# Kernel optimization log

Hardware: AMD Instinct MI355X
Metric: run time of the kernel (lower is better)

The kernel has to match this reference:

```python
import jax, jax.numpy as jnp
import numpy as np

D = 768; NH = 12; HD = D // NH; L = 12; NC = 27; PATCH = 16; MLP = 3072; PROJ = 512
IMG = 224; GRID = IMG // PATCH; HW = GRID * GRID; S = NC + HW
NEG = -1e9

def _ln(x, w, b):
    m = jnp.mean(x, -1, keepdims=True)
    v = jnp.mean(jnp.square(x - m), -1, keepdims=True)
    return (x - m) * jax.lax.rsqrt(v + 1e-5) * w + b

def _quick_gelu(x):
    return x * jax.nn.sigmoid(1.702 * x)

def _build_mask(attn_obj_masks, dtype):
    # CRIS block mask: cls<->cls blocked except self; cls->patch allowed only for
    # patches of that class; patch->cls blocked; patch->patch fully allowed.
    B = attn_obj_masks.shape[0]
    oh = jax.nn.one_hot(attn_obj_masks, NC, dtype=dtype)              # [B, HW, NC]
    T11 = jnp.broadcast_to(1.0 - jnp.eye(NC, dtype=dtype), (B, NC, NC))
    M13 = 1.0 - jnp.swapaxes(oh, 1, 2)                                # [B, NC, HW]
    top = jnp.concatenate([T11, M13], axis=2)
    bot = jnp.concatenate([jnp.ones((B, HW, NC), dtype), jnp.zeros((B, HW, HW), dtype)], axis=2)
    Mb = jnp.concatenate([top, bot], axis=1)                          # [B, S, S]
    return jnp.where(Mb == 1.0, jnp.asarray(NEG, dtype), jnp.asarray(0.0, dtype))

def reference(img, sents, attn_obj_masks, obj_masks, cls_tokens, patch_w, patch_b, pos_embed,
              ln1_w, ln1_b, qkv_w, qkv_b, out_w, out_b, ln2_w, ln2_b,
              mlp_w1, mlp_b1, mlp_w2, mlp_b2, ln_post_w, ln_post_b, proj):
    B = img.shape[0]
    sents = sents / jnp.linalg.norm(sents, axis=-1, keepdims=True)    # encode_text output, L2 normed
    mask = _build_mask(attn_obj_masks, img.dtype)                     # [B, S, S]
    # patch embedding (conv stride 16) -> [B, HW, D]
    p = jax.lax.conv_general_dilated(img, patch_w, (PATCH, PATCH), 'VALID',
                                     dimension_numbers=('NCHW', 'OIHW', 'NCHW'))
    p = p.reshape(B, D, HW).transpose(0, 2, 1) + patch_b
    x = jnp.concatenate([jnp.broadcast_to(cls_tokens, (B, NC, D)), p], axis=1) + pos_embed
    scale = 1.0 / np.sqrt(HD).astype(np.float32)
    def block(x, prm):
        l1w, l1b, qw, qb, ow, ob, l2w, l2b, w1, b1, w2, b2 = prm
        h = _ln(x, l1w, l1b)
        qkv = h @ qw + qb
        q, k, v = jnp.split(qkv, 3, axis=-1)
        q = q.reshape(B, S, NH, HD).transpose(0, 2, 1, 3)
        k = k.reshape(B, S, NH, HD).transpose(0, 2, 1, 3)
        v = v.reshape(B, S, NH, HD).transpose(0, 2, 1, 3)
        scores = jnp.einsum('bhqd,bhkd->bhqk', q, k) * scale + mask[:, None]
        a = jax.nn.softmax(scores, axis=-1)
        o = jnp.einsum('bhqk,bhkd->bhqd', a, v).transpose(0, 2, 1, 3).reshape(B, S, D)
        x = x + o @ ow + ob
        h = _ln(x, l2w, l2b)
        x = x + _quick_gelu(h @ w1 + b1) @ w2 + b2
        return x, None
    x, _ = jax.lax.scan(block, x, (ln1_w, ln1_b, qkv_w, qkv_b, out_w, out_b,
                                   ln2_w, ln2_b, mlp_w1, mlp_b1, mlp_w2, mlp_b2))
    tokens = _ln(x, ln_post_w, ln_post_b) @ proj                      # [B, S, PROJ]
    obj = tokens[:, :NC]
    obj = obj / jnp.linalg.norm(obj, axis=-1, keepdims=True)
    pred_id = jnp.einsum('bnd,bd->bn', obj, sents)                    # [B, NC]
    # per-class scatter loop == gather of pred_id by per-pixel class id
    pred = jnp.take_along_axis(pred_id, obj_masks.reshape(B, -1), axis=1).reshape(obj_masks.shape)
    return pred                                                       # [B, 224, 224]

def setup_inputs():
    B = 16; std = 0.02
    ks = jax.random.split(jax.random.key(0), 16)
    f = jax.random.normal
    return {
        'img': f(ks[0], (B, 3, IMG, IMG), jnp.float32),
        'sents': f(ks[1], (B, PROJ), jnp.float32),
        'attn_obj_masks': jax.random.randint(ks[2], (B, HW), 0, NC, jnp.int32),
        'obj_masks': jax.random.randint(ks[3], (B, IMG, IMG), 0, NC, jnp.int32),
        'cls_tokens': f(ks[4], (1, NC, D)) * std,
        'patch_w': f(ks[5], (D, 3, PATCH, PATCH)) * std,
        'patch_b': jnp.zeros((D,)),
        'pos_embed': f(ks[6], (S, D)) * std,
        'ln1_w': jnp.ones((L, D)), 'ln1_b': jnp.zeros((L, D)),
        'qkv_w': f(ks[7], (L, D, 3 * D)) * std, 'qkv_b': jnp.zeros((L, 3 * D)),
        'out_w': f(ks[8], (L, D, D)) * std, 'out_b': jnp.zeros((L, D)),
        'ln2_w': jnp.ones((L, D)), 'ln2_b': jnp.zeros((L, D)),
        'mlp_w1': f(ks[9], (L, D, MLP)) * std, 'mlp_b1': jnp.zeros((L, MLP)),
        'mlp_w2': f(ks[10], (L, MLP, D)) * std, 'mlp_b2': jnp.zeros((L, D)),
        'ln_post_w': jnp.ones((D,)), 'ln_post_b': jnp.zeros((D,)),
        'proj': f(ks[11], (D, PROJ)) * std,
    }
```

## Files before the change

kernel.cpp:

```cpp
#include <hip/hip_runtime.h>

#define DEV __device__ __forceinline__

typedef short bf16x8 __attribute__((ext_vector_type(8)));
typedef float f32x4 __attribute__((ext_vector_type(4)));
typedef int vi4 __attribute__((ext_vector_type(4)));
typedef unsigned short u16;
typedef short short4v __attribute__((ext_vector_type(4)));

#define NEGV -1000000000.0f

DEV u16 f2bf(float f) {
  union { float f; unsigned u; } v; v.f = f;
  unsigned r = v.u + 0x7FFFu + ((v.u >> 16) & 1u);
  return (u16)(r >> 16);
}

DEV bf16x8 ld_bf8(const u16* p) {
  vi4 v = *(const vi4*)p;
  return __builtin_bit_cast(bf16x8, v);
}

DEV void gload_lds16(const u16* g, vi4* l) {
  __builtin_amdgcn_global_load_lds((const __attribute__((address_space(1))) void*)g,
                                   (__attribute__((address_space(3))) void*)l, 16, 0, 0);
}

template<int BN, int MODE, bool GELU, int KS>
__global__ __launch_bounds__(256) void gemm_bt(
    const u16* __restrict__ A, const u16* __restrict__ Bt,
    const float* __restrict__ bias,
    float* __restrict__ Cf, u16* __restrict__ Cb,
    int M, int N, int K, const float* __restrict__ pos)
{
  constexpr int FJ = BN / 32;
  constexpr int LTOT = 4 + FJ;
  __shared__ vi4 As[2][1024];
  __shared__ vi4 Bs[2][BN * 8];

  int gx = gridDim.x, gy = gridDim.y;
  int nwg = gx * gy * (int)gridDim.z;
  int orig = blockIdx.x + gx * (blockIdx.y + gy * blockIdx.z);
  int qq = nwg >> 3, rr = nwg & 7;
  int xcd = orig & 7, off = orig >> 3;
  int id = (xcd < rr) ? xcd * (qq + 1) + off : rr * (qq + 1) + (xcd - rr) * qq + off;
  int bx = id % gx, rest = id / gx, by = rest % gy, bz = rest / gy;

  int tid = threadIdx.x, lane = tid & 63, wid = tid >> 6;
  int wm = wid >> 1, wn = wid & 1;
  int m0 = by * 128, n0 = bx * BN;
  int kBeg = (K / KS) * bz;
  int nT = (K / KS) >> 6;
  f32x4 acc[4][FJ] = {};

  auto STAGE = [&](int buf, int kk) {
    #pragma unroll
    for (int r = 0; r < 4; ++r) {
      int flat = r * 256 + tid;
      int row = flat >> 3, c = flat & 7;
      int cs = c ^ (row & 7);
      gload_lds16(A + (long)(m0 + row) * K + kk + cs * 8, &As[buf][r * 256 + wid * 64]);
    }
    #pragma unroll
    for (int r = 0; r < FJ; ++r) {
      int flat = r * 256 + tid;
      int row = flat >> 3, c = flat & 7;
      int cs = c ^ (row & 7);
      gload_lds16(Bt + (long)(n0 + row) * K + kk + cs * 8, &Bs[buf][r * 256 + wid * 64]);
    }
  };

  STAGE(0, kBeg);
  int cur = 0;
  for (int t = 0; t < nT; ++t) {
    if (t + 1 < nT) {
      STAGE(cur ^ 1, kBeg + (t + 1) * 64);
      asm volatile("s_waitcnt vmcnt(%0)" :: "i"(LTOT) : "memory");
    } else {
      asm volatile("s_waitcnt vmcnt(0)" ::: "memory");
    }
    __builtin_amdgcn_s_barrier();
    int cg = lane >> 4, l15 = lane & 15;
    #pragma unroll
    for (int ks = 0; ks < 2; ++ks) {
      bf16x8 af[4], bfr[FJ];
      #pragma unroll
      for (int i = 0; i < 4; ++i) {
        int ra = wm * 64 + i * 16 + l15;
        af[i] = __builtin_bit_cast(bf16x8, As[cur][ra * 8 + ((ks * 4 + cg) ^ (ra & 7))]);
      }
      #pragma unroll
      for (int j = 0; j < FJ; ++j) {
        int rb = wn * (BN / 2) + j * 16 + l15;
        bfr[j] = __builtin_bit_cast(bf16x8, Bs[cur][rb * 8 + ((ks * 4 + cg) ^ (rb & 7))]);
      }
      #pragma unroll
      for (int i = 0; i < 4; ++i)
        #pragma unroll
        for (int j = 0; j < FJ; ++j)
          acc[i][j] = __builtin_amdgcn_mfma_f32_16x16x32_bf16(af[i], bfr[j], acc[i][j], 0, 0, 0);
    }
    __builtin_amdgcn_s_barrier();
    cur ^= 1;
  }

  int cg = lane >> 4, l15 = lane & 15;
  #pragma unroll
  for (int i = 0; i < 4; ++i) {
    #pragma unroll
    for (int j = 0; j < FJ; ++j) {
      int col = n0 + wn * (BN / 2) + j * 16 + l15;
      float bv = bias ? bias[col] : 0.f;
      #pragma unroll
      for (int r = 0; r < 4; ++r) {
        int row = m0 + wm * 64 + i * 16 + cg * 4 + r;
        if (row < M) {
          float v = acc[i][j][r];
          if (KS == 1 || bz == 0) v += bv;
          if (GELU) v = v / (1.f + __expf(-1.702f * v));
          if (MODE == 0) Cb[(long)row * N + col] = f2bf(v);
          else if (MODE == 1) {
            if (KS > 1) atomicAdd(&Cf[(long)row * N + col], v);
            else Cf[(long)row * N + col] += v;
          }
          else if (MODE == 2) Cf[(long)row * N + col] = v;
          else {
            int hw = row % 196;
            int xr = (row / 196) * 223 + 27 + hw;
            Cf[(long)xr * 768 + col] = v + pos[(27 + hw) * 768 + col];
          }
        }
      }
    }
  }
}

__global__ __launch_bounds__(256) void attn_kernel(
    const u16* __restrict__ QKV, const int* __restrict__ aom, u16* __restrict__ O)
{
  __shared__ vi4 Kl[224 * 8];
  __shared__ vi4 Vt[64 * 28];
  __shared__ vi4 Pl[4][16 * 28];
  __shared__ int ml[196];
  int tid = threadIdx.x, lane = tid & 63, wid = tid >> 6;
  int qg = blockIdx.x, h = blockIdx.y, b = blockIdx.z;
  long rowbase = (long)b * 223;
  #pragma unroll
  for (int it = 0; it < 7; ++it) {
    int flat = it * 256 + tid;
    int s = flat >> 3, c = flat & 7;
    int cs = c ^ (s & 7);
    gload_lds16(QKV + (rowbase + s) * 2304 + 768 + h * 64 + cs * 8, &Kl[it * 256 + wid * 64]);
  }
  u16* vt16 = (u16*)Vt;
  #pragma unroll
  for (int it = 0; it < 7; ++it) {
    int flat = it * 256 + tid;
    int s = flat >> 3, c = flat & 7;
    vi4 v = {0, 0, 0, 0};
    if (s < 223) v = *(const vi4*)(QKV + (rowbase + s) * 2304 + 1536 + h * 64 + c * 8);
    union { vi4 v4; u16 hx[8]; } uu; uu.v4 = v;
    int cs = s >> 3;
    #pragma unroll
    for (int j = 0; j < 8; ++j) {
      int d = c * 8 + j;
      vt16[d * 224 + (cs ^ ((d >> 1) & 3)) * 8 + (s & 7)] = uu.hx[j];
    }
  }
  for (int i = tid; i < 196; i += 256) ml[i] = aom[b * 196 + i];
  __syncthreads();

  int colk = lane & 15, cg = lane >> 4;
  #pragma unroll
  for (int rep = 0; rep < 2; ++rep) {
    int fo = wid * 2 + rep;
    if (fo >= 7) break;
    int qf = qg * 7 + fo;
    int q0 = qf * 16;
    int arow = q0 + colk; if (arow > 222) arow = 222;
    const u16* qb = QKV + (rowbase + arow) * 2304 + h * 64;
    bf16x8 aq0 = ld_bf8(qb + cg * 8);
    bf16x8 aq1 = ld_bf8(qb + 32 + cg * 8);

    f32x4 sc[14];
    #pragma unroll
    for (int kf = 0; kf < 14; ++kf) {
      int key = kf * 16 + colk;
      f32x4 a = {0.f, 0.f, 0.f, 0.f};
      bf16x8 bk0 = __builtin_bit_cast(bf16x8, Kl[key * 8 + (cg ^ (key & 7))]);
      bf16x8 bk1 = __builtin_bit_cast(bf16x8, Kl[key * 8 + ((4 + cg) ^ (key & 7))]);
      a = __builtin_amdgcn_mfma_f32_16x16x32_bf16(aq0, bk0, a, 0, 0, 0);
      a = __builtin_amdgcn_mfma_f32_16x16x32_bf16(aq1, bk1, a, 0, 0, 0);
      sc[kf] = a;
    }
    #pragma unroll
    for (int r = 0; r < 4; ++r) {
      int q = q0 + cg * 4 + r;
      float mx = -3.4e38f;
      #pragma unroll
      for (int kf = 0; kf < 14; ++kf) {
        int key = kf * 16 + colk;
        float mval;
        if (key >= 223) mval = NEGV;
        else if (q >= 27) mval = (key < 27) ? NEGV : 0.f;
        else if (key < 27) mval = (key == q) ? 0.f : NEGV;
        else mval = (ml[key - 27] == q) ? 0.f : NEGV;
        float s = sc[kf][r] * 0.125f + mval;
        sc[kf][r] = s;
        mx = fmaxf(mx, s);
      }
      #pragma unroll
      for (int d = 1; d < 16; d <<= 1) mx = fmaxf(mx, __shfl_xor(mx, d));
      float sum = 0.f;
      #pragma unroll
      for (int kf = 0; kf < 14; ++kf) {
        float e = __expf(sc[kf][r] - mx);
        sc[kf][r] = e; sum += e;
      }
      #pragma unroll
      for (int d = 1; d < 16; d <<= 1) sum += __shfl_xor(sum, d);
      float inv = 1.f / sum;
      #pragma unroll
      for (int kf = 0; kf < 14; ++kf) sc[kf][r] *= inv;
    }
    u16* pw = (u16*)Pl[wid];
    #pragma unroll
    for (int kf = 0; kf < 14; ++kf) {
      int key = kf * 16 + colk;
      int ck = key >> 3;
      #pragma unroll
      for (int r = 0; r < 4; ++r) {
        int prow = cg * 4 + r;
        pw[prow * 224 + (ck ^ ((prow >> 1) & 3)) * 8 + (key & 7)] = f2bf(sc[kf][r]);
      }
    }
    f32x4 oacc[4] = {};
    #pragma unroll
    for (int ks = 0; ks < 7; ++ks) {
      bf16x8 pa = __builtin_bit_cast(bf16x8, Pl[wid][colk * 28 + ((ks * 4 + cg) ^ ((colk >> 1) & 3))]);
      #pragma unroll
      for (int nf = 0; nf < 4; ++nf) {
        int d = nf * 16 + colk;
        bf16x8 bv = __builtin_bit_cast(bf16x8, Vt[d * 28 + ((ks * 4 + cg) ^ ((d >> 1) & 3))]);
        oacc[nf] = __builtin_amdgcn_mfma_f32_16x16x32_bf16(pa, bv, oacc[nf], 0, 0, 0);
      }
    }
    #pragma unroll
    for (int nf = 0; nf < 4; ++nf) {
      int d = h * 64 + nf * 16 + colk;
      #pragma unroll
      for (int r = 0; r < 4; ++r) {
        int q = q0 + cg * 4 + r;
        if (q < 223) O[(rowbase + q) * 768 + d] = f2bf(oacc[nf][r]);
      }
    }
  }
}

template<bool MAP27>
__global__ __launch_bounds__(256) void ln_kernel(
    const float* __restrict__ X, u16* __restrict__ Hb,
    const float* __restrict__ w, const float* __restrict__ bb, int nrows)
{
  int row = blockIdx.x * 4 + (threadIdx.x >> 6);
  if (row >= nrows) return;
  int xr = MAP27 ? (row / 27) * 223 + (row % 27) : row;
  int l = threadIdx.x & 63;
  const float4* xp = (const float4*)(X + (long)xr * 768);
  float4 a = xp[l], c = xp[l + 64], d = xp[l + 128];
  float s = a.x + a.y + a.z + a.w + c.x + c.y + c.z + c.w + d.x + d.y + d.z + d.w;
  #pragma unroll
  for (int t = 1; t < 64; t <<= 1) s += __shfl_xor(s, t);
  float mean = s * (1.f / 768.f);
  a.x -= mean; a.y -= mean; a.z -= mean; a.w -= mean;
  c.x -= mean; c.y -= mean; c.z -= mean; c.w -= mean;
  d.x -= mean; d.y -= mean; d.z -= mean; d.w -= mean;
  float q = a.x*a.x + a.y*a.y + a.z*a.z + a.w*a.w
          + c.x*c.x + c.y*c.y + c.z*c.z + c.w*c.w
          + d.x*d.x + d.y*d.y + d.z*d.z + d.w*d.w;
  #pragma unroll
  for (int t = 1; t < 64; t <<= 1) q += __shfl_xor(q, t);
  float rs = rsqrtf(q * (1.f / 768.f) + 1e-5f);
  const float4* wp = (const float4*)w;
  const float4* bp = (const float4*)bb;
  u16* out = Hb + (long)row * 768;
  float4 w0 = wp[l], w1 = wp[l + 64], w2 = wp[l + 128];
  float4 b0 = bp[l], b1 = bp[l + 64], b2 = bp[l + 128];
  short4v o;
  o[0] = (short)f2bf(a.x * rs * w0.x + b0.x); o[1] = (short)f2bf(a.y * rs * w0.y + b0.y);
  o[2] = (short)f2bf(a.z * rs * w0.z + b0.z); o[3] = (short)f2bf(a.w * rs * w0.w + b0.w);
  *(short4v*)(out + l * 4) = o;
  o[0] = (short)f2bf(c.x * rs * w1.x + b1.x); o[1] = (short)f2bf(c.y * rs * w1.y + b1.y);
  o[2] = (short)f2bf(c.z * rs * w1.z + b1.z); o[3] = (short)f2bf(c.w * rs * w1.w + b1.w);
  *(short4v*)(out + 256 + l * 4) = o;
  o[0] = (short)f2bf(d.x * rs * w2.x + b2.x); o[1] = (short)f2bf(d.y * rs * w2.y + b2.y);
  o[2] = (short)f2bf(d.z * rs * w2.z + b2.z); o[3] = (short)f2bf(d.w * rs * w2.w + b2.w);
  *(short4v*)(out + 512 + l * 4) = o;
}

__global__ __launch_bounds__(256) void transpose_w(
    const float* __restrict__ W, u16* __restrict__ WT, int K, int N, long sW, long sT)
{
  __shared__ float t[64][65];
  int z = blockIdx.z;
  W += (long)z * sW; WT += (long)z * sT;
  int n0 = blockIdx.x * 64, k0 = blockIdx.y * 64;
  #pragma unroll
  for (int i = 0; i < 4; ++i) {
    int flat = i * 256 + threadIdx.x;
    int r = flat >> 4, c = (flat & 15) * 4;
    float4 v = *(const float4*)(W + (long)(k0 + r) * N + n0 + c);
    t[r][c] = v.x; t[r][c + 1] = v.y; t[r][c + 2] = v.z; t[r][c + 3] = v.w;
  }
  __syncthreads();
  #pragma unroll
  for (int i = 0; i < 8; ++i) {
    int flat = i * 256 + threadIdx.x;
    int rn = flat >> 5, ck = (flat & 31) * 2;
    unsigned val = (unsigned)f2bf(t[ck][rn]) | ((unsigned)f2bf(t[ck + 1][rn]) << 16);
    *(unsigned*)(WT + (long)(n0 + rn) * K + k0 + ck) = val;
  }
}

__global__ void convert_bf16(const float* __restrict__ src, u16* __restrict__ dst, int n) {
  int i = blockIdx.x * 256 + threadIdx.x;
  if (i < n) dst[i] = f2bf(src[i]);
}

__global__ __launch_bounds__(192) void patch_extract(const float* __restrict__ img, u16* __restrict__ Xp) {
  int row = blockIdx.x;
  int t = threadIdx.x;
  int pair = t >> 2, part = t & 3;
  int cch = pair >> 4, kh = pair & 15;
  int b = row / 196, hw = row % 196, gh = hw / 14, gw = hw % 14;
  float4 v = *(const float4*)(img + ((long)(b * 3 + cch) * 224 + gh * 16 + kh) * 224 + gw * 16 + part * 4);
  short4v o;
  o[0] = (short)f2bf(v.x); o[1] = (short)f2bf(v.y); o[2] = (short)f2bf(v.z); o[3] = (short)f2bf(v.w);
  *(short4v*)(Xp + (long)row * 768 + pair * 16 + part * 4) = o;
}

__global__ void cls_pos_fill(const float* __restrict__ cls, const float* __restrict__ pos, float* __restrict__ x) {
  int i = blockIdx.x * 256 + threadIdx.x;
  if (i >= 16 * 27 * 768) return;
  int d = i % 768, t = i / 768, b = t / 27, s = t % 27;
  x[((long)b * 223 + s) * 768 + d] = cls[s * 768 + d] + pos[s * 768 + d];
}

__global__ __launch_bounds__(256) void sents_norm(const float* __restrict__ s, float* __restrict__ sn) {
  __shared__ float sb[4];
  int b = blockIdx.x, t = threadIdx.x;
  float v0 = s[b * 512 + t], v1 = s[b * 512 + t + 256];
  float q = v0 * v0 + v1 * v1;
  #pragma unroll
  for (int d = 1; d < 64; d <<= 1) q += __shfl_xor(q, d);
  if ((t & 63) == 0) sb[t >> 6] = q;
  __syncthreads();
  float inv = rsqrtf(sb[0] + sb[1] + sb[2] + sb[3]);
  sn[b * 512 + t] = v0 * inv;
  sn[b * 512 + t + 256] = v1 * inv;
}

__global__ __launch_bounds__(256) void obj_dot(const float* __restrict__ obj, const float* __restrict__ sn, float* __restrict__ pid) {
  __shared__ float sb[8];
  int r = blockIdx.x, t = threadIdx.x, b = r / 27;
  float v0 = obj[(long)r * 512 + t], v1 = obj[(long)r * 512 + t + 256];
  float w0 = sn[b * 512 + t], w1 = sn[b * 512 + t + 256];
  float q = v0 * v0 + v1 * v1;
  float dt = v0 * w0 + v1 * w1;
  #pragma unroll
  for (int d = 1; d < 64; d <<= 1) { q += __shfl_xor(q, d); dt += __shfl_xor(dt, d); }
  if ((t & 63) == 0) { sb[t >> 6] = q; sb[4 + (t >> 6)] = dt; }
  __syncthreads();
  if (t == 0) pid[r] = (sb[4] + sb[5] + sb[6] + sb[7]) * rsqrtf(sb[0] + sb[1] + sb[2] + sb[3]);
}

__global__ void gather_pred(const int* __restrict__ om, const float* __restrict__ pid, float* __restrict__ out) {
  int i = blockIdx.x * 256 + threadIdx.x;
  if (i >= 16 * 224 * 224) return;
  int b = i / (224 * 224);
  out[i] = pid[b * 27 + om[i]];
}

extern "C" void kernel_launch(void* const* d_in, const int* in_sizes, int n_in,
                              void* d_out, int out_size, void* d_ws, size_t ws_size,
                              hipStream_t stream) {
  const float* img     = (const float*)d_in[0];
  const float* sents   = (const float*)d_in[1];
  const int*   aom     = (const int*)d_in[2];
  const int*   omask   = (const int*)d_in[3];
  const float* cls     = (const float*)d_in[4];
  const float* patch_w = (const float*)d_in[5];
  const float* patch_b = (const float*)d_in[6];
  const float* pos     = (const float*)d_in[7];
  const float* ln1w    = (const float*)d_in[8];
  const float* ln1b    = (const float*)d_in[9];
  const float* qkvw    = (const float*)d_in[10];
  const float* qkvb    = (const float*)d_in[11];
  const float* outw    = (const float*)d_in[12];
  const float* outb    = (const float*)d_in[13];
  const float* ln2w    = (const float*)d_in[14];
  const float* ln2b    = (const float*)d_in[15];
  const float* m1w     = (const float*)d_in[16];
  const float* m1b     = (const float*)d_in[17];
  const float* m2w     = (const float*)d_in[18];
  const float* m2b     = (const float*)d_in[19];
  const float* lnpw    = (const float*)d_in[20];
  const float* lnpb    = (const float*)d_in[21];
  const float* projw   = (const float*)d_in[22];

  char* p = (char*)d_ws;
  auto alloc = [&](size_t bytes) { char* r = p; p += (bytes + 255) & ~(size_t)255; return r; };
  float* x   = (float*)alloc(3568ul * 768 * 4);
  u16* H     = (u16*)alloc(3584ul * 768 * 2);
  u16* QKV   = (u16*)alloc(3584ul * 2304 * 2);
  u16* Obuf  = (u16*)alloc(3584ul * 768 * 2);
  u16* G     = (u16*)alloc(3584ul * 3072 * 2);
  u16* PWc   = (u16*)alloc(768ul * 768 * 2);
  u16* PrT   = (u16*)alloc(512ul * 768 * 2);
  float* obj = (float*)alloc(432ul * 512 * 4);
  float* sn  = (float*)alloc(16ul * 512 * 4);
  float* pid = (float*)alloc(432ul * 4);

  const size_t wlayer = (2304ul * 768 + 768ul * 768 + 3072ul * 768 + 768ul * 3072) * 2;
  size_t used = (size_t)(p - (char*)d_ws);
  int nw = (ws_size >= used + 12 * wlayer + 65536) ? 12 : 1;
  const long sQ = 2304l * 768, sO = 768l * 768, s1 = 768l * 3072, s2 = 3072l * 768;
  u16* WqT = (u16*)alloc((size_t)sQ * 2 * nw);
  u16* WoT = (u16*)alloc((size_t)sO * 2 * nw);
  u16* W1T = (u16*)alloc((size_t)s1 * 2 * nw);
  u16* W2T = (u16*)alloc((size_t)s2 * 2 * nw);

  convert_bf16<<<2304, 256, 0, stream>>>(patch_w, PWc, 768 * 768);
  transpose_w<<<dim3(8, 12, 1), 256, 0, stream>>>(projw, PrT, 768, 512, 0, 0);
  if (nw == 12) {
    transpose_w<<<dim3(36, 12, 12), 256, 0, stream>>>(qkvw, WqT, 768, 2304, sQ, sQ);
    transpose_w<<<dim3(12, 12, 12), 256, 0, stream>>>(outw, WoT, 768, 768, sO, sO);
    transpose_w<<<dim3(48, 12, 12), 256, 0, stream>>>(m1w, W1T, 768, 3072, s1, s1);
    transpose_w<<<dim3(12, 48, 12), 256, 0, stream>>>(m2w, W2T, 3072, 768, s2, s2);
  }
  patch_extract<<<3136, 192, 0, stream>>>(img, H);
  cls_pos_fill<<<1296, 256, 0, stream>>>(cls, pos, x);
  gemm_bt<64, 3, false, 1><<<dim3(12, 25), 256, 0, stream>>>(H, PWc, patch_b, x, nullptr, 3136, 768, 768, pos);

  for (int l = 0; l < 12; ++l) {
    u16 *wq, *wo, *w1, *w2;
    if (nw == 12) { wq = WqT + (long)l * sQ; wo = WoT + (long)l * sO; w1 = W1T + (long)l * s1; w2 = W2T + (long)l * s2; }
    else {
      wq = WqT; wo = WoT; w1 = W1T; w2 = W2T;
      transpose_w<<<dim3(36, 12, 1), 256, 0, stream>>>(qkvw + (long)l * sQ, wq, 768, 2304, 0, 0);
      transpose_w<<<dim3(12, 12, 1), 256, 0, stream>>>(outw + (long)l * sO, wo, 768, 768, 0, 0);
      transpose_w<<<dim3(48, 12, 1), 256, 0, stream>>>(m1w + (long)l * s1, w1, 768, 3072, 0, 0);
      transpose_w<<<dim3(12, 48, 1), 256, 0, stream>>>(m2w + (long)l * s2, w2, 3072, 768, 0, 0);
    }
    ln_kernel<false><<<892, 256, 0, stream>>>(x, H, ln1w + l * 768, ln1b + l * 768, 3568);
    gemm_bt<128, 0, false, 1><<<dim3(18, 28), 256, 0, stream>>>(H, wq, qkvb + l * 2304, nullptr, QKV, 3568, 2304, 768, nullptr);
    attn_kernel<<<dim3(2, 12, 16), 256, 0, stream>>>(QKV, aom, Obuf);
    gemm_bt<64, 1, false, 2><<<dim3(12, 28, 2), 256, 0, stream>>>(Obuf, wo, outb + l * 768, x, nullptr, 3568, 768, 768, nullptr);
    ln_kernel<false><<<892, 256, 0, stream>>>(x, H, ln2w + l * 768, ln2b + l * 768, 3568);
    gemm_bt<128, 0, true, 1><<<dim3(24, 28), 256, 0, stream>>>(H, w1, m1b + l * 3072, nullptr, G, 3568, 3072, 768, nullptr);
    gemm_bt<64, 1, false, 2><<<dim3(12, 28, 2), 256, 0, stream>>>(G, w2, m2b + l * 768, x, nullptr, 3568, 768, 3072, nullptr);
  }

  ln_kernel<true><<<108, 256, 0, stream>>>(x, H, lnpw, lnpb, 432);
  hipMemsetAsync(obj, 0, 432ul * 512 * 4, stream);
  gemm_bt<64, 1, false, 2><<<dim3(8, 4, 2), 256, 0, stream>>>(H, PrT, nullptr, obj, nullptr, 432, 512, 768, nullptr);
  sents_norm<<<16, 256, 0, stream>>>(sents, sn);
  obj_dot<<<432, 256, 0, stream>>>(obj, sn, pid);
  gather_pred<<<3136, 256, 0, stream>>>(omask, pid, (float*)d_out);
}
```

Measured before the change: 2.479 ms.

## Replace split-K atomic accumulation with partial buffers reduced inside layernorm

The split-K output-projection and MLP-down GEMMs now write plain stores of their two K-partials into separate fp32 buffers instead of doing atomicAdd or read-modify-write into the residual stream. The following layernorm kernel sums the residual with both partials, writes the updated residual back, and normalizes it in the same pass. The final projection GEMM drops split-K and the memset. This removes atomic traffic and the read-modify-write on x, at the cost of two extra fp32 partial buffers and more reads in layernorm.

```diff
diff --git a/kernel.cpp b/kernel.cpp
--- a/kernel.cpp
+++ b/kernel.cpp
@@ -31,7 +31,7 @@
     const u16* __restrict__ A, const u16* __restrict__ Bt,
     const float* __restrict__ bias,
     float* __restrict__ Cf, u16* __restrict__ Cb,
-    int M, int N, int K, const float* __restrict__ pos)
+    int M, int N, int K, const float* __restrict__ pos, long pstride)
 {
   constexpr int FJ = BN / 32;
   constexpr int LTOT = 4 + FJ;
@@ -105,6 +105,7 @@
   }
 
   int cg = lane >> 4, l15 = lane & 15;
+  float* Cfz = (MODE == 2 && KS > 1) ? Cf + (long)bz * pstride : Cf;
   #pragma unroll
   for (int i = 0; i < 4; ++i) {
     #pragma unroll
@@ -119,11 +120,7 @@
           if (KS == 1 || bz == 0) v += bv;
           if (GELU) v = v / (1.f + __expf(-1.702f * v));
           if (MODE == 0) Cb[(long)row * N + col] = f2bf(v);
-          else if (MODE == 1) {
-            if (KS > 1) atomicAdd(&Cf[(long)row * N + col], v);
-            else Cf[(long)row * N + col] += v;
-          }
-          else if (MODE == 2) Cf[(long)row * N + col] = v;
+          else if (MODE == 2) Cfz[(long)row * N + col] = v;
           else {
             int hw = row % 196;
             int xr = (row / 196) * 223 + 27 + hw;
@@ -257,9 +254,10 @@
   }
 }
 
-template<bool MAP27>
+template<int NADD, bool MAP27, bool WRITEX>
 __global__ __launch_bounds__(256) void ln_kernel(
-    const float* __restrict__ X, u16* __restrict__ Hb,
+    const float* __restrict__ X, const float* __restrict__ P, long ps,
+    float* __restrict__ Xout, u16* __restrict__ Hb,
     const float* __restrict__ w, const float* __restrict__ bb, int nrows)
 {
   int row = blockIdx.x * 4 + (threadIdx.x >> 6);
@@ -268,6 +266,19 @@
   int l = threadIdx.x & 63;
   const float4* xp = (const float4*)(X + (long)xr * 768);
   float4 a = xp[l], c = xp[l + 64], d = xp[l + 128];
+  if (NADD == 2) {
+    const float4* p0 = (const float4*)(P + (long)xr * 768);
+    const float4* p1 = (const float4*)(P + ps + (long)xr * 768);
+    float4 u0 = p0[l], u1 = p0[l + 64], u2 = p0[l + 128];
+    float4 v0 = p1[l], v1 = p1[l + 64], v2 = p1[l + 128];
+    a.x += u0.x + v0.x; a.y += u0.y + v0.y; a.z += u0.z + v0.z; a.w += u0.w + v0.w;
+    c.x += u1.x + v1.x; c.y += u1.y + v1.y; c.z += u1.z + v1.z; c.w += u1.w + v1.w;
+    d.x += u2.x + v2.x; d.y += u2.y + v2.y; d.z += u2.z + v2.z; d.w += u2.w + v2.w;
+  }
+  if (WRITEX) {
+    float4* xo = (float4*)(Xout + (long)xr * 768);
+    xo[l] = a; xo[l + 64] = c; xo[l + 128] = d;
+  }
   float s = a.x + a.y + a.z + a.w + c.x + c.y + c.z + c.w + d.x + d.y + d.z + d.w;
   #pragma unroll
   for (int t = 1; t < 64; t <<= 1) s += __shfl_xor(s, t);
@@ -410,11 +421,14 @@
 
   char* p = (char*)d_ws;
   auto alloc = [&](size_t bytes) { char* r = p; p += (bytes + 255) & ~(size_t)255; return r; };
+  const long PS = 3584l * 768;
   float* x   = (float*)alloc(3568ul * 768 * 4);
   u16* H     = (u16*)alloc(3584ul * 768 * 2);
   u16* QKV   = (u16*)alloc(3584ul * 2304 * 2);
   u16* Obuf  = (u16*)alloc(3584ul * 768 * 2);
   u16* G     = (u16*)alloc(3584ul * 3072 * 2);
+  float* Y   = (float*)alloc((size_t)PS * 2 * 4);
+  float* Mp  = (float*)alloc((size_t)PS * 2 * 4);
   u16* PWc   = (u16*)alloc(768ul * 768 * 2);
   u16* PrT   = (u16*)alloc(512ul * 768 * 2);
   float* obj = (float*)alloc(432ul * 512 * 4);
@@ -440,7 +454,7 @@
   }
   patch_extract<<<3136, 192, 0, stream>>>(img, H);
   cls_pos_fill<<<1296, 256, 0, stream>>>(cls, pos, x);
-  gemm_bt<64, 3, false, 1><<<dim3(12, 25), 256, 0, stream>>>(H, PWc, patch_b, x, nullptr, 3136, 768, 768, pos);
+  gemm_bt<64, 3, false, 1><<<dim3(12, 25), 256, 0, stream>>>(H, PWc, patch_b, x, nullptr, 3136, 768, 768, pos, 0);
 
   for (int l = 0; l < 12; ++l) {
     u16 *wq, *wo, *w1, *w2;
@@ -452,18 +466,20 @@
       transpose_w<<<dim3(48, 12, 1), 256, 0, stream>>>(m1w + (long)l * s1, w1, 768, 3072, 0, 0);
       transpose_w<<<dim3(12, 48, 1), 256, 0, stream>>>(m2w + (long)l * s2, w2, 3072, 768, 0, 0);
     }
-    ln_kernel<false><<<892, 256, 0, stream>>>(x, H, ln1w + l * 768, ln1b + l * 768, 3568);
-    gemm_bt<128, 0, false, 1><<<dim3(18, 28), 256, 0, stream>>>(H, wq, qkvb + l * 2304, nullptr, QKV, 3568, 2304, 768, nullptr);
+    if (l == 0)
+      ln_kernel<0, false, false><<<892, 256, 0, stream>>>(x, nullptr, 0, nullptr, H, ln1w, ln1b, 3568);
+    else
+      ln_kernel<2, false, true><<<892, 256, 0, stream>>>(x, Mp, PS, x, H, ln1w + l * 768, ln1b + l * 768, 3568);
+    gemm_bt<128, 0, false, 1><<<dim3(18, 28), 256, 0, stream>>>(H, wq, qkvb + l * 2304, nullptr, QKV, 3568, 2304, 768, nullptr, 0);
     attn_kernel<<<dim3(2, 12, 16), 256, 0, stream>>>(QKV, aom, Obuf);
-    gemm_bt<64, 1, false, 2><<<dim3(12, 28, 2), 256, 0, stream>>>(Obuf, wo, outb + l * 768, x, nullptr, 3568, 768, 768, nullptr);
-    ln_kernel<false><<<892, 256, 0, stream>>>(x, H, ln2w + l * 768, ln2b + l * 768, 3568);
-    gemm_bt<128, 0, true, 1><<<dim3(24, 28), 256, 0, stream>>>(H, w1, m1b + l * 3072, nullptr, G, 3568, 3072, 768, nullptr);
-    gemm_bt<64, 1, false, 2><<<dim3(12, 28, 2), 256, 0, stream>>>(G, w2, m2b + l * 768, x, nullptr, 3568, 768, 3072, nullptr);
-  }
-
-  ln_kernel<true><<<108, 256, 0, stream>>>(x, H, lnpw, lnpb, 432);
-  hipMemsetAsync(obj, 0, 432ul * 512 * 4, stream);
-  gemm_bt<64, 1, false, 2><<<dim3(8, 4, 2), 256, 0, stream>>>(H, PrT, nullptr, obj, nullptr, 432, 512, 768, nullptr);
+    gemm_bt<64, 2, false, 2><<<dim3(12, 28, 2), 256, 0, stream>>>(Obuf, wo, outb + l * 768, Y, nullptr, 3568, 768, 768, nullptr, PS);
+    ln_kernel<2, false, true><<<892, 256, 0, stream>>>(x, Y, PS, x, H, ln2w + l * 768, ln2b + l * 768, 3568);
+    gemm_bt<128, 0, true, 1><<<dim3(24, 28), 256, 0, stream>>>(H, w1, m1b + l * 3072, nullptr, G, 3568, 3072, 768, nullptr, 0);
+    gemm_bt<64, 2, false, 2><<<dim3(12, 28, 2), 256, 0, stream>>>(G, w2, m2b + l * 768, Mp, nullptr, 3568, 768, 3072, nullptr, PS);
+  }
+
+  ln_kernel<2, true, false><<<108, 256, 0, stream>>>(x, Mp, PS, nullptr, H, lnpw, lnpb, 432);
+  gemm_bt<64, 2, false, 1><<<dim3(8, 4), 256, 0, stream>>>(H, PrT, nullptr, obj, nullptr, 432, 512, 768, nullptr, 0);
   sents_norm<<<16, 256, 0, stream>>>(sents, sn);
   obj_dot<<<432, 256, 0, stream>>>(obj, sn, pid);
   gather_pred<<<3136, 256, 0, stream>>>(omask, pid, (float*)d_out);
```

Result: faster. 2.377 ms (-4.1%).
